# Kernel tuning notes

Hardware: AMD Instinct MI355X
Metric: run time of the kernel (lower is better)

## Reference

```python
import jax, jax.numpy as jnp
import numpy as np

B, S, E, A, DK, H = 8, 2048, 256, 16, 64, 64  # batch, seq, embed, action, d_key, mlp hidden


def setup_inputs() -> dict:
    key = jax.random.key(0)
    ks = jax.random.split(key, 8)
    obs = jax.random.normal(ks[0], (B, S, E), dtype=jnp.float32)
    act = jnp.zeros((B, S, A), dtype=jnp.float32)  # one-hot actions; unused by forward
    # projection weights stored as [in, out] (torch Linear applies x @ W.T)
    Wq = jax.random.normal(ks[1], (E, DK), dtype=jnp.float32) / np.sqrt(E)
    Wk = jax.random.normal(ks[2], (E, DK), dtype=jnp.float32) / np.sqrt(E)
    Wv = jax.random.normal(ks[3], (E, DK), dtype=jnp.float32) / np.sqrt(E)
    W1 = jax.random.normal(ks[4], (DK, H), dtype=jnp.float32) / np.sqrt(DK)
    b1 = jnp.zeros((H,), dtype=jnp.float32)
    W2 = jax.random.normal(ks[5], (H, 1), dtype=jnp.float32) / np.sqrt(H)
    b2 = jnp.zeros((1,), dtype=jnp.float32)
    return dict(obs=obs, act=act, Wq=Wq, Wk=Wk, Wv=Wv, W1=W1, b1=b1, W2=W2, b2=b2)


def reference(obs, act, Wq, Wk, Wv, W1, b1, W2, b2):
    b, s, _ = obs.shape
    dk = Wq.shape[1]
    scale = dk ** -0.25  # applied to both q and k, net 1/sqrt(dk)
    q = (obs @ Wq) * scale          # [b, s, dk]
    k = (obs @ Wk) * scale          # [b, s, dk]
    v = obs @ Wv                    # [b, s, dk]
    scores = jnp.einsum('bqd,bkd->bqk', q, k)  # [b, s, s]
    causal = jnp.tril(jnp.ones((s, s), dtype=bool))
    scores = jnp.where(causal[None], scores, -jnp.inf)
    attn = jax.nn.softmax(scores, axis=2)      # [b, s, s]
    attn_out = jnp.einsum('bqk,bkd->bqd', attn, v)  # [b, s, dk]
    h = jax.nn.relu(attn_out.reshape(b * s, dk) @ W1 + b1)
    x = h @ W2 + b2                 # [b*s, 1]
    return (x, attn)
```

## Files before the change

kernel.cpp:

```cpp
#include <hip/hip_runtime.h>
#include <hip/hip_bf16.h>
#include <math.h>

#define NB 8
#define SQ 2048
#define NSP 4

typedef __attribute__((ext_vector_type(8))) short short8;
typedef __attribute__((ext_vector_type(4))) float f32x4;

__device__ __forceinline__ short f2bf(float f) {
    union { float f; unsigned u; } v; v.f = f;
    unsigned r = v.u + 0x7FFF + ((v.u >> 16) & 1);
    return (short)(r >> 16);
}

__global__ __launch_bounds__(256) void k_wt(const float* __restrict__ Wq,
                                            const float* __restrict__ Wk,
                                            const float* __restrict__ Wv,
                                            short* __restrict__ wt) {
    int o = blockIdx.x * 256 + threadIdx.x;
    int row = o >> 8, e = o & 255;
    int w = row >> 6, d = row & 63;
    const float* W = (w == 0) ? Wq : ((w == 1) ? Wk : Wv);
    wt[o] = f2bf(W[e * 64 + d]);
}

__global__ __launch_bounds__(256, 4) void k_proj(const float* __restrict__ obs,
                                                 const short* __restrict__ wt,
                                                 short* __restrict__ qw,
                                                 short* __restrict__ kw,
                                                 short* __restrict__ vt) {
    int tid = threadIdx.x, w = tid >> 6, l = tid & 63, lg = l >> 4, lc = l & 15;
    int r0 = blockIdx.x * 16;
    int arow = r0 + lc;
    f32x4 accq = {0.f,0.f,0.f,0.f}, acck = {0.f,0.f,0.f,0.f}, accv = {0.f,0.f,0.f,0.f};
    const short* wq = wt + (size_t)(w * 16 + lc) * 256;
    const short* wk = wt + (size_t)(64 + w * 16 + lc) * 256;
    const short* wv = wt + (size_t)(128 + w * 16 + lc) * 256;
    #pragma unroll
    for (int ks = 0; ks < 8; ++ks) {
        int e0 = ks * 32 + lg * 8;
        const float* ap = obs + (size_t)arow * 256 + e0;
        float4 f0 = *(const float4*)ap;
        float4 f1 = *(const float4*)(ap + 4);
        short8 a;
        a[0] = f2bf(f0.x); a[1] = f2bf(f0.y); a[2] = f2bf(f0.z); a[3] = f2bf(f0.w);
        a[4] = f2bf(f1.x); a[5] = f2bf(f1.y); a[6] = f2bf(f1.z); a[7] = f2bf(f1.w);
        accq = __builtin_amdgcn_mfma_f32_16x16x32_bf16(a, *(const short8*)(wq + e0), accq, 0, 0, 0);
        acck = __builtin_amdgcn_mfma_f32_16x16x32_bf16(a, *(const short8*)(wk + e0), acck, 0, 0, 0);
        accv = __builtin_amdgcn_mfma_f32_16x16x32_bf16(a, *(const short8*)(wv + e0), accv, 0, 0, 0);
    }
    const float scale = 0.35355339059327373f;
    __shared__ short ldsv[64][18];
    #pragma unroll
    for (int r = 0; r < 4; ++r) {
        int row = r0 + lg * 4 + r;
        qw[(size_t)row * 64 + w * 16 + lc] = f2bf(accq[r] * scale);
        kw[(size_t)row * 64 + w * 16 + lc] = f2bf(acck[r] * scale);
        ldsv[w * 16 + lc][lg * 4 + r] = f2bf(accv[r]);
    }
    __syncthreads();
    int b = r0 >> 11, s0 = r0 & 2047;
    int d = tid >> 2, sc = (tid & 3) * 4;
    short* dst = vt + (size_t)b * 64 * SQ + (size_t)d * SQ + s0 + sc;
    dst[0] = ldsv[d][sc]; dst[1] = ldsv[d][sc + 1];
    dst[2] = ldsv[d][sc + 2]; dst[3] = ldsv[d][sc + 3];
}

__global__ __launch_bounds__(256) void k_flash(const short* __restrict__ qw,
                                               const short* __restrict__ kw,
                                               const short* __restrict__ vt,
                                               float* __restrict__ op,
                                               float* __restrict__ lpart,
                                               float* __restrict__ attn) {
    int qb = blockIdx.x, sp = blockIdx.y, b = blockIdx.z;
    if (sp > qb) return;
    int q0 = qb * 64;
    int tid = threadIdx.x, w = tid >> 6, l = tid & 63, lg = l >> 4, lc = l & 15;
    int r0 = q0 + w * 16;
    int eo = lg * 8;
    __shared__ short ldsP[4][16][72];
    const short* qbase = qw + (size_t)b * SQ * 64;
    const short* kbase = kw + (size_t)b * SQ * 64;
    const short* vbase = vt + (size_t)b * 64 * SQ;
    float* abase = attn + (size_t)b * SQ * SQ;
    short8 qf0 = *(const short8*)(qbase + (size_t)(r0 + lc) * 64 + eo);
    short8 qf1 = *(const short8*)(qbase + (size_t)(r0 + lc) * 64 + 32 + eo);
    float lsum[4];
    f32x4 o[4];
    #pragma unroll
    for (int r = 0; r < 4; ++r) lsum[r] = 0.f;
    #pragma unroll
    for (int nj = 0; nj < 4; ++nj) o[nj] = (f32x4){0.f, 0.f, 0.f, 0.f};

    for (int kb = sp; kb <= qb; kb += NSP) {
        int k0 = kb * 64;
        f32x4 s[4];
        #pragma unroll
        for (int nj = 0; nj < 4; ++nj) s[nj] = (f32x4){0.f, 0.f, 0.f, 0.f};
        #pragma unroll
        for (int nj = 0; nj < 4; ++nj) {
            short8 kf = *(const short8*)(kbase + (size_t)(k0 + nj * 16 + lc) * 64 + eo);
            s[nj] = __builtin_amdgcn_mfma_f32_16x16x32_bf16(qf0, kf, s[nj], 0, 0, 0);
        }
        #pragma unroll
        for (int nj = 0; nj < 4; ++nj) {
            short8 kf = *(const short8*)(kbase + (size_t)(k0 + nj * 16 + lc) * 64 + 32 + eo);
            s[nj] = __builtin_amdgcn_mfma_f32_16x16x32_bf16(qf1, kf, s[nj], 0, 0, 0);
        }
        if (kb == qb) {
            #pragma unroll
            for (int nj = 0; nj < 4; ++nj)
                #pragma unroll
                for (int r = 0; r < 4; ++r)
                    if (k0 + nj * 16 + lc > r0 + lg * 4 + r) s[nj][r] = -INFINITY;
        }
        #pragma unroll
        for (int r = 0; r < 4; ++r) {
            int row = r0 + lg * 4 + r;
            float ps = 0.f;
            #pragma unroll
            for (int nj = 0; nj < 4; ++nj) {
                float p = __expf(s[nj][r]);
                ps += p;
                ldsP[w][lg * 4 + r][nj * 16 + lc] = f2bf(p);
                abase[(size_t)row * SQ + k0 + nj * 16 + lc] = p;
            }
            ps += __shfl_xor(ps, 1);
            ps += __shfl_xor(ps, 2);
            ps += __shfl_xor(ps, 4);
            ps += __shfl_xor(ps, 8);
            lsum[r] += ps;
        }
        #pragma unroll
        for (int ks = 0; ks < 2; ++ks) {
            short8 pa = *(const short8*)&ldsP[w][lc][ks * 32 + lg * 8];
            #pragma unroll
            for (int nj = 0; nj < 4; ++nj) {
                short8 vf = *(const short8*)(vbase + (size_t)(nj * 16 + lc) * SQ + k0 + ks * 32 + eo);
                o[nj] = __builtin_amdgcn_mfma_f32_16x16x32_bf16(pa, vf, o[nj], 0, 0, 0);
            }
        }
    }
    size_t pb = ((size_t)sp * NB + b) * SQ;
    #pragma unroll
    for (int r = 0; r < 4; ++r) {
        int row = r0 + lg * 4 + r;
        if (lc == 0) lpart[pb + row] = lsum[r];
        #pragma unroll
        for (int nj = 0; nj < 4; ++nj)
            op[(pb + row) * 64 + nj * 16 + lc] = o[nj][r];
    }
}

__global__ __launch_bounds__(256) void k_lred(const float* __restrict__ lpart,
                                              float* __restrict__ linv) {
    int g = blockIdx.x * 256 + threadIdx.x;
    int s = g & 2047, b = g >> 11;
    int nsp = (s >> 6) + 1; if (nsp > NSP) nsp = NSP;
    float t = 0.f;
    for (int sp = 0; sp < nsp; ++sp) t += lpart[((size_t)sp * NB + b) * SQ + s];
    linv[g] = 1.f / t;
}

__global__ __launch_bounds__(256) void k_combine(const float* __restrict__ op,
                                                 const float* __restrict__ linv,
                                                 const float* __restrict__ W1,
                                                 const float* __restrict__ b1,
                                                 const float* __restrict__ W2,
                                                 const float* __restrict__ b2,
                                                 float* __restrict__ x) {
    int row0 = blockIdx.x * 8;
    int tid = threadIdx.x, w = tid >> 6, l = tid & 63;
    __shared__ float w1l[64][64];
    __shared__ float aol[8][64];
    {
        const float4* src = (const float4*)W1;
        float4* dst = (float4*)&w1l[0][0];
        #pragma unroll
        for (int i = 0; i < 4; ++i) dst[tid + i * 256] = src[tid + i * 256];
    }
    #pragma unroll
    for (int rr = 0; rr < 2; ++rr) {
        int grow = row0 + w * 2 + rr;
        int b = grow >> 11, s = grow & 2047;
        int nsp = (s >> 6) + 1; if (nsp > NSP) nsp = NSP;
        float od = 0.f;
        for (int sp = 0; sp < nsp; ++sp)
            od += op[(((size_t)sp * NB + b) * SQ + s) * 64 + l];
        aol[w * 2 + rr][l] = od * linv[grow];
    }
    __syncthreads();
    #pragma unroll
    for (int rr = 0; rr < 2; ++rr) {
        int grow = row0 + w * 2 + rr;
        float t = b1[l];
        #pragma unroll 16
        for (int d = 0; d < 64; ++d) t += aol[w * 2 + rr][d] * w1l[d][l];
        float h = fmaxf(t, 0.f);
        float px = h * W2[l];
        px += __shfl_xor(px, 1);
        px += __shfl_xor(px, 2);
        px += __shfl_xor(px, 4);
        px += __shfl_xor(px, 8);
        px += __shfl_xor(px, 16);
        px += __shfl_xor(px, 32);
        if (l == 0) x[grow] = px + b2[0];
    }
}

__global__ __launch_bounds__(256) void k_scale(const float* __restrict__ linv,
                                               float* __restrict__ attn) {
    int csp = blockIdx.x, qb = blockIdx.y, b = blockIdx.z;
    int tid = threadIdx.x, w = tid >> 6, l = tid & 63;
    float* abase = attn + (size_t)b * SQ * SQ;
    int colb = csp * 256 + l * 4;
    if (csp * 4 > qb) {
        float4 z = {0.f, 0.f, 0.f, 0.f};
        #pragma unroll
        for (int r = 0; r < 16; ++r) {
            int row = qb * 64 + w * 16 + r;
            *(float4*)(abase + (size_t)row * SQ + colb) = z;
        }
        return;
    }
    #pragma unroll
    for (int r = 0; r < 16; ++r) {
        int row = qb * 64 + w * 16 + r;
        float inv = linv[(size_t)b * SQ + row];
        int lim = row | 63;
        float* p = abase + (size_t)row * SQ + colb;
        float4 v = *(const float4*)p;
        float4 o;
        o.x = (colb + 0 <= lim) ? v.x * inv : 0.f;
        o.y = (colb + 1 <= lim) ? v.y * inv : 0.f;
        o.z = (colb + 2 <= lim) ? v.z * inv : 0.f;
        o.w = (colb + 3 <= lim) ? v.w * inv : 0.f;
        *(float4*)p = o;
    }
}

extern "C" void kernel_launch(void* const* d_in, const int* in_sizes, int n_in,
                              void* d_out, int out_size, void* d_ws, size_t ws_size,
                              hipStream_t stream) {
    const float* obs = (const float*)d_in[0];
    const float* Wq  = (const float*)d_in[2];
    const float* Wk  = (const float*)d_in[3];
    const float* Wv  = (const float*)d_in[4];
    const float* W1  = (const float*)d_in[5];
    const float* b1  = (const float*)d_in[6];
    const float* W2  = (const float*)d_in[7];
    const float* b2  = (const float*)d_in[8];

    float* x    = (float*)d_out;
    float* attn = (float*)d_out + NB * SQ;

    char* ws = (char*)d_ws;
    short* wt    = (short*)(ws);
    short* qw    = (short*)(ws + 131072);
    short* kw    = (short*)(ws + 2228224);
    short* vt    = (short*)(ws + 4325376);
    float* lpart = (float*)(ws + 6422528);
    float* linv  = (float*)(ws + 6684672);
    float* op    = (float*)(ws + 6750208);

    k_wt<<<dim3(192), dim3(256), 0, stream>>>(Wq, Wk, Wv, wt);
    k_proj<<<dim3(1024), dim3(256), 0, stream>>>(obs, wt, qw, kw, vt);
    k_flash<<<dim3(32, NSP, NB), dim3(256), 0, stream>>>(qw, kw, vt, op, lpart, attn);
    k_lred<<<dim3(64), dim3(256), 0, stream>>>(lpart, linv);
    k_combine<<<dim3(2048), dim3(256), 0, stream>>>(op, linv, W1, b1, W2, b2, x);
    k_scale<<<dim3(8, 32, NB), dim3(256), 0, stream>>>(linv, attn);
}
```

Baseline: 140.4 us.

## Stage unnormalized probabilities in bf16 scratch and write attn once

The flash kernel now stores unnormalized probabilities as bf16 into a workspace buffer instead of fp32 into the output, and the final kernel reads that buffer, scales by the inverse row sum and writes attn once. This removes the fp32 read-modify-write pass over the output. The separate row-sum reduction kernel is folded into the combine kernel, the split count doubles, and the partial outputs now live in the attn output region as scratch. The cost is bf16 rounding of the attention values, and the scratch buffer must fit in the workspace.

Result: no change. 143.0 us (+1.9%).

```diff
diff --git a/kernel.cpp b/kernel.cpp
--- a/kernel.cpp
+++ b/kernel.cpp
@@ -4,7 +4,7 @@
 
 #define NB 8
 #define SQ 2048
-#define NSP 4
+#define NSP 8
 
 typedef __attribute__((ext_vector_type(8))) short short8;
 typedef __attribute__((ext_vector_type(4))) float f32x4;
@@ -13,6 +13,10 @@
     union { float f; unsigned u; } v; v.f = f;
     unsigned r = v.u + 0x7FFF + ((v.u >> 16) & 1);
     return (short)(r >> 16);
+}
+__device__ __forceinline__ float bf2f(short s) {
+    union { unsigned u; float f; } v; v.u = ((unsigned)(unsigned short)s) << 16;
+    return v.f;
 }
 
 __global__ __launch_bounds__(256) void k_wt(const float* __restrict__ Wq,
@@ -73,7 +77,7 @@
                                                const short* __restrict__ vt,
                                                float* __restrict__ op,
                                                float* __restrict__ lpart,
-                                               float* __restrict__ attn) {
+                                               short* __restrict__ pbuf) {
     int qb = blockIdx.x, sp = blockIdx.y, b = blockIdx.z;
     if (sp > qb) return;
     int q0 = qb * 64;
@@ -84,7 +88,7 @@
     const short* qbase = qw + (size_t)b * SQ * 64;
     const short* kbase = kw + (size_t)b * SQ * 64;
     const short* vbase = vt + (size_t)b * 64 * SQ;
-    float* abase = attn + (size_t)b * SQ * SQ;
+    short* pbase = pbuf + (size_t)b * SQ * SQ;
     short8 qf0 = *(const short8*)(qbase + (size_t)(r0 + lc) * 64 + eo);
     short8 qf1 = *(const short8*)(qbase + (size_t)(r0 + lc) * 64 + 32 + eo);
     float lsum[4];
@@ -118,14 +122,12 @@
         }
         #pragma unroll
         for (int r = 0; r < 4; ++r) {
-            int row = r0 + lg * 4 + r;
             float ps = 0.f;
             #pragma unroll
             for (int nj = 0; nj < 4; ++nj) {
                 float p = __expf(s[nj][r]);
                 ps += p;
                 ldsP[w][lg * 4 + r][nj * 16 + lc] = f2bf(p);
-                abase[(size_t)row * SQ + k0 + nj * 16 + lc] = p;
             }
             ps += __shfl_xor(ps, 1);
             ps += __shfl_xor(ps, 2);
@@ -136,6 +138,7 @@
         #pragma unroll
         for (int ks = 0; ks < 2; ++ks) {
             short8 pa = *(const short8*)&ldsP[w][lc][ks * 32 + lg * 8];
+            *(short8*)(pbase + (size_t)(r0 + lc) * SQ + k0 + ks * 32 + lg * 8) = pa;
             #pragma unroll
             for (int nj = 0; nj < 4; ++nj) {
                 short8 vf = *(const short8*)(vbase + (size_t)(nj * 16 + lc) * SQ + k0 + ks * 32 + eo);
@@ -154,23 +157,14 @@
     }
 }
 
-__global__ __launch_bounds__(256) void k_lred(const float* __restrict__ lpart,
-                                              float* __restrict__ linv) {
-    int g = blockIdx.x * 256 + threadIdx.x;
-    int s = g & 2047, b = g >> 11;
-    int nsp = (s >> 6) + 1; if (nsp > NSP) nsp = NSP;
-    float t = 0.f;
-    for (int sp = 0; sp < nsp; ++sp) t += lpart[((size_t)sp * NB + b) * SQ + s];
-    linv[g] = 1.f / t;
-}
-
 __global__ __launch_bounds__(256) void k_combine(const float* __restrict__ op,
-                                                 const float* __restrict__ linv,
+                                                 const float* __restrict__ lpart,
                                                  const float* __restrict__ W1,
                                                  const float* __restrict__ b1,
                                                  const float* __restrict__ W2,
                                                  const float* __restrict__ b2,
-                                                 float* __restrict__ x) {
+                                                 float* __restrict__ x,
+                                                 float* __restrict__ linv) {
     int row0 = blockIdx.x * 8;
     int tid = threadIdx.x, w = tid >> 6, l = tid & 63;
     __shared__ float w1l[64][64];
@@ -186,10 +180,15 @@
         int grow = row0 + w * 2 + rr;
         int b = grow >> 11, s = grow & 2047;
         int nsp = (s >> 6) + 1; if (nsp > NSP) nsp = NSP;
-        float od = 0.f;
-        for (int sp = 0; sp < nsp; ++sp)
-            od += op[(((size_t)sp * NB + b) * SQ + s) * 64 + l];
-        aol[w * 2 + rr][l] = od * linv[grow];
+        float od = 0.f, lt = 0.f;
+        for (int sp = 0; sp < nsp; ++sp) {
+            size_t base = (size_t)(sp * NB + b) * SQ + s;
+            od += op[base * 64 + l];
+            lt += lpart[base];
+        }
+        float inv = 1.f / lt;
+        aol[w * 2 + rr][l] = od * inv;
+        if (l == 0) linv[grow] = inv;
     }
     __syncthreads();
     #pragma unroll
@@ -210,13 +209,17 @@
     }
 }
 
-__global__ __launch_bounds__(256) void k_scale(const float* __restrict__ linv,
+__global__ __launch_bounds__(256) void k_write(const short* __restrict__ pbuf,
+                                               const float* __restrict__ linv,
                                                float* __restrict__ attn) {
     int csp = blockIdx.x, qb = blockIdx.y, b = blockIdx.z;
     int tid = threadIdx.x, w = tid >> 6, l = tid & 63;
+    __shared__ float liv[64];
+    if (tid < 64) liv[tid] = linv[(size_t)b * SQ + qb * 64 + tid];
+    __syncthreads();
     float* abase = attn + (size_t)b * SQ * SQ;
     int colb = csp * 256 + l * 4;
-    if (csp * 4 > qb) {
+    if ((colb >> 6) > qb) {
         float4 z = {0.f, 0.f, 0.f, 0.f};
         #pragma unroll
         for (int r = 0; r < 16; ++r) {
@@ -225,19 +228,18 @@
         }
         return;
     }
+    const short* pbase = pbuf + (size_t)b * SQ * SQ;
     #pragma unroll
     for (int r = 0; r < 16; ++r) {
         int row = qb * 64 + w * 16 + r;
-        float inv = linv[(size_t)b * SQ + row];
-        int lim = row | 63;
-        float* p = abase + (size_t)row * SQ + colb;
-        float4 v = *(const float4*)p;
+        float inv = liv[w * 16 + r];
+        short4 pv = *(const short4*)(pbase + (size_t)row * SQ + colb);
         float4 o;
-        o.x = (colb + 0 <= lim) ? v.x * inv : 0.f;
-        o.y = (colb + 1 <= lim) ? v.y * inv : 0.f;
-        o.z = (colb + 2 <= lim) ? v.z * inv : 0.f;
-        o.w = (colb + 3 <= lim) ? v.w * inv : 0.f;
-        *(float4*)p = o;
+        o.x = bf2f(pv.x) * inv;
+        o.y = bf2f(pv.y) * inv;
+        o.z = bf2f(pv.z) * inv;
+        o.w = bf2f(pv.w) * inv;
+        *(float4*)(abase + (size_t)row * SQ + colb) = o;
     }
 }
 
@@ -256,19 +258,20 @@
     float* x    = (float*)d_out;
     float* attn = (float*)d_out + NB * SQ;
 
+    float* op = attn;
+
     char* ws = (char*)d_ws;
     short* wt    = (short*)(ws);
     short* qw    = (short*)(ws + 131072);
     short* kw    = (short*)(ws + 2228224);
     short* vt    = (short*)(ws + 4325376);
     float* lpart = (float*)(ws + 6422528);
-    float* linv  = (float*)(ws + 6684672);
-    float* op    = (float*)(ws + 6750208);
+    float* linv  = (float*)(ws + 6946816);
+    short* pbuf  = (short*)(ws + 7012352);
 
     k_wt<<<dim3(192), dim3(256), 0, stream>>>(Wq, Wk, Wv, wt);
     k_proj<<<dim3(1024), dim3(256), 0, stream>>>(obs, wt, qw, kw, vt);
-    k_flash<<<dim3(32, NSP, NB), dim3(256), 0, stream>>>(qw, kw, vt, op, lpart, attn);
-    k_lred<<<dim3(64), dim3(256), 0, stream>>>(lpart, linv);
-    k_combine<<<dim3(2048), dim3(256), 0, stream>>>(op, linv, W1, b1, W2, b2, x);
-    k_scale<<<dim3(8, 32, NB), dim3(256), 0, stream>>>(linv, attn);
-}
+    k_flash<<<dim3(32, NSP, NB), dim3(256), 0, stream>>>(qw, kw, vt, op, lpart, pbuf);
+    k_combine<<<dim3(2048), dim3(256), 0, stream>>>(op, lpart, W1, b1, W2, b2, x, linv);
+    k_write<<<dim3(8, 32, NB), dim3(256), 0, stream>>>(pbuf, linv, attn);
+}
```
